# Performance work log

Measured on AMD Instinct MI355X. Metric: run time of the kernel, lower is better.

Reference implementation:

```python
import jax, jax.numpy as jnp
import numpy as np
import math

E = 64    # d_model = 2*feats
FF = 16   # dim_feedforward
F = 32    # feats
W = 100   # window_size
B = 128   # batch
NH = 32   # nhead = feats


def _mha(q_in, kv_in, w_qkv, b_qkv, w_o, b_o):
    # PyTorch nn.MultiheadAttention, seq-first layout [L, B, E]
    wq, wk, wv = jnp.split(w_qkv, 3, axis=0)
    bq, bk, bv = jnp.split(b_qkv, 3)
    q = q_in @ wq.T + bq
    k = kv_in @ wk.T + bk
    v = kv_in @ wv.T + bv
    L, Bb, _ = q.shape
    S = k.shape[0]
    hd = E // NH  # head_dim = 2
    qh = q.reshape(L, Bb, NH, hd)
    kh = k.reshape(S, Bb, NH, hd)
    vh = v.reshape(S, Bb, NH, hd)
    scores = jnp.einsum('lbhd,sbhd->bhls', qh, kh) / math.sqrt(hd)
    attn = jax.nn.softmax(scores, axis=-1)
    out = jnp.einsum('bhls,sbhd->lbhd', attn, vh).reshape(L, Bb, E)
    return out @ w_o.T + b_o


def _ffn(x, w1, b1, w2, b2):
    h = x @ w1.T + b1
    # nn.LeakyReLU(True) => negative_slope=True==1.0 => identity activation
    return h @ w2.T + b2


def _pos_encode(x):
    # pe[t,d] = sin(t*div[d]) + cos(t*div[d])  (both added, as in source)
    div = jnp.exp(jnp.arange(E, dtype=x.dtype) * (-math.log(10000.0) / E))
    pos = jnp.arange(x.shape[0], dtype=x.dtype)[:, None]
    pe = jnp.sin(pos * div) + jnp.cos(pos * div)  # [W, E]
    return x + pe[:, None, :]


def _encode(src, c, tgt, enc_p):
    (qkv_w, qkv_b, out_w, out_b, l1_w, l1_b, l2_w, l2_b) = enc_p
    s = jnp.concatenate([src, c], axis=2) * math.sqrt(F)
    s = _pos_encode(s)
    s = s + _mha(s, s, qkv_w, qkv_b, out_w, out_b)
    s = s + _ffn(s, l1_w, l1_b, l2_w, l2_b)
    t = jnp.tile(tgt, (1, 1, 2))
    return t, s


def _decode(t, mem, dec_p):
    (sa_qkv_w, sa_qkv_b, sa_out_w, sa_out_b,
     ca_qkv_w, ca_qkv_b, ca_out_w, ca_out_b,
     l1_w, l1_b, l2_w, l2_b) = dec_p
    t = t + _mha(t, t, sa_qkv_w, sa_qkv_b, sa_out_w, sa_out_b)
    t = t + _mha(t, mem, ca_qkv_w, ca_qkv_b, ca_out_w, ca_out_b)
    t = t + _ffn(t, l1_w, l1_b, l2_w, l2_b)
    return t


def _forward(src, tgt,
             enc_qkv_w, enc_qkv_b, enc_out_w, enc_out_b, enc_l1_w, enc_l1_b, enc_l2_w, enc_l2_b,
             d1_sa_qkv_w, d1_sa_qkv_b, d1_sa_out_w, d1_sa_out_b,
             d1_ca_qkv_w, d1_ca_qkv_b, d1_ca_out_w, d1_ca_out_b,
             d1_l1_w, d1_l1_b, d1_l2_w, d1_l2_b,
             d2_sa_qkv_w, d2_sa_qkv_b, d2_sa_out_w, d2_sa_out_b,
             d2_ca_qkv_w, d2_ca_qkv_b, d2_ca_out_w, d2_ca_out_b,
             d2_l1_w, d2_l1_b, d2_l2_w, d2_l2_b,
             fcn_w, fcn_b):
    enc_p = (enc_qkv_w, enc_qkv_b, enc_out_w, enc_out_b, enc_l1_w, enc_l1_b, enc_l2_w, enc_l2_b)
    d1_p = (d1_sa_qkv_w, d1_sa_qkv_b, d1_sa_out_w, d1_sa_out_b,
            d1_ca_qkv_w, d1_ca_qkv_b, d1_ca_out_w, d1_ca_out_b,
            d1_l1_w, d1_l1_b, d1_l2_w, d1_l2_b)
    d2_p = (d2_sa_qkv_w, d2_sa_qkv_b, d2_sa_out_w, d2_sa_out_b,
            d2_ca_qkv_w, d2_ca_qkv_b, d2_ca_out_w, d2_ca_out_b,
            d2_l1_w, d2_l1_b, d2_l2_w, d2_l2_b)
    fcn = lambda x: jax.nn.sigmoid(x @ fcn_w.T + fcn_b)

    c = jnp.zeros_like(src)
    t, mem = _encode(src, c, tgt, enc_p)
    x1 = fcn(_decode(t, mem, d1_p))
    c = (x1 - src) ** 2
    t, mem = _encode(src, c, tgt, enc_p)
    x2 = fcn(_decode(t, mem, d2_p))
    return x1, x2


def setup_inputs() -> dict:
    keys = jax.random.split(jax.random.key(0), 40)
    ki = iter(keys)

    def rn(shape, s=0.05):
        return jax.random.normal(next(ki), shape, dtype=jnp.float32) * s

    inp = {}
    inp['src'] = jax.random.normal(next(ki), (W, B, F), dtype=jnp.float32)
    inp['tgt'] = jax.random.normal(next(ki), (W, B, F), dtype=jnp.float32)
    for pfx in ['enc_', 'd1_sa_', 'd1_ca_', 'd2_sa_', 'd2_ca_']:
        inp[pfx + 'qkv_w'] = rn((3 * E, E))
        inp[pfx + 'qkv_b'] = rn((3 * E,))
        inp[pfx + 'out_w'] = rn((E, E))
        inp[pfx + 'out_b'] = rn((E,))
    for pfx in ['enc_', 'd1_', 'd2_']:
        inp[pfx + 'l1_w'] = rn((FF, E))
        inp[pfx + 'l1_b'] = rn((FF,))
        inp[pfx + 'l2_w'] = rn((E, FF))
        inp[pfx + 'l2_b'] = rn((E,))
    inp['fcn_w'] = rn((F, E))
    inp['fcn_b'] = rn((F,))
    return inp


def reference(src, tgt,
              enc_qkv_w, enc_qkv_b, enc_out_w, enc_out_b, enc_l1_w, enc_l1_b, enc_l2_w, enc_l2_b,
              d1_sa_qkv_w, d1_sa_qkv_b, d1_sa_out_w, d1_sa_out_b,
              d1_ca_qkv_w, d1_ca_qkv_b, d1_ca_out_w, d1_ca_out_b,
              d1_l1_w, d1_l1_b, d1_l2_w, d1_l2_b,
              d2_sa_qkv_w, d2_sa_qkv_b, d2_sa_out_w, d2_sa_out_b,
              d2_ca_qkv_w, d2_ca_qkv_b, d2_ca_out_w, d2_ca_out_b,
              d2_l1_w, d2_l1_b, d2_l2_w, d2_l2_b,
              fcn_w, fcn_b):
    return _forward(src, tgt,
                    enc_qkv_w, enc_qkv_b, enc_out_w, enc_out_b, enc_l1_w, enc_l1_b, enc_l2_w, enc_l2_b,
                    d1_sa_qkv_w, d1_sa_qkv_b, d1_sa_out_w, d1_sa_out_b,
                    d1_ca_qkv_w, d1_ca_qkv_b, d1_ca_out_w, d1_ca_out_b,
                    d1_l1_w, d1_l1_b, d1_l2_w, d1_l2_b,
                    d2_sa_qkv_w, d2_sa_qkv_b, d2_sa_out_w, d2_sa_out_b,
                    d2_ca_qkv_w, d2_ca_qkv_b, d2_ca_out_w, d2_ca_out_b,
                    d2_l1_w, d2_l1_b, d2_l2_w, d2_l2_b,
                    fcn_w, fcn_b)
```

## Files before the change

kernel.cpp:

```cpp
#include <hip/hip_runtime.h>
#include <math.h>


#define TPB 1024
#define RH 50
#define SQ32 5.656854249492381f

#ifndef __has_builtin
#define __has_builtin(x) 0
#endif
#if __has_builtin(__builtin_amdgcn_exp2f)
#define EXP2(x) __builtin_amdgcn_exp2f(x)
#else
#define EXP2(x) exp2f(x)
#endif

typedef float v2f __attribute__((ext_vector_type(2)));
typedef float v4f __attribute__((ext_vector_type(4)));

struct KParams { const void* p[36]; };

template<int K, int MC, int WP>
__device__ __forceinline__ void ldwp(const float* __restrict__ Wt, float* __restrict__ Ws,
                                     int moff, int tid)
{
    for (int i = tid; i < MC * K; i += TPB) {
        int m = i / K, k = i - m * K;
        Ws[k * WP + moff + m] = Wt[i];
    }
}

template<int K, int WP>
__device__ __forceinline__ void gemm_dual24(const float* __restrict__ x0,
                                            const float* __restrict__ x1,
                                            const float* __restrict__ w, v2f acc[4])
{
#pragma unroll 4
    for (int kk = 0; kk < K / 4; ++kk) {
        v4f xa = *reinterpret_cast<const v4f*>(x0 + 4 * kk);
        v4f xb = *reinterpret_cast<const v4f*>(x1 + 4 * kk);
#pragma unroll
        for (int j = 0; j < 4; ++j) {
            v4f wv = *reinterpret_cast<const v4f*>(w + (size_t)(4 * kk + j) * WP);
            v2f xj = {xa[j], xb[j]};
#pragma unroll
            for (int c = 0; c < 4; ++c) {
                v2f wc = {wv[c], wv[c]};
                acc[c] = __builtin_elementwise_fma(xj, wc, acc[c]);
            }
        }
    }
}

template<int K, int WP>
__device__ __forceinline__ void gemm14v(const float* __restrict__ x,
                                        const float* __restrict__ w, float acc[4])
{
#pragma unroll 4
    for (int kk = 0; kk < K / 4; ++kk) {
        v4f xv = *reinterpret_cast<const v4f*>(x + 4 * kk);
#pragma unroll
        for (int j = 0; j < 4; ++j) {
            v4f wv = *reinterpret_cast<const v4f*>(w + (size_t)(4 * kk + j) * WP);
#pragma unroll
            for (int c = 0; c < 4; ++c) acc[c] = fmaf(xv[j], wv[c], acc[c]);
        }
    }
}

__device__ __forceinline__ void kv_gemm(const float* __restrict__ Xkv,
    const float* __restrict__ RW, const float* __restrict__ Bqkv,
    int b, int base, float4* __restrict__ KVs, float4* __restrict__ Gx, int tid)
{
    if (tid >= 800) return;
    const int isV = tid >= 400;
    const int u = tid - (isV ? 400 : 0);
    const int r0 = u >> 4, cg = u & 15;
    v2f acc[4] = {};
    gemm_dual24<64, 132>(Xkv + r0 * 68, Xkv + (r0 + 25) * 68,
                         RW + (isV ? 64 : 0) + 4 * cg, acc);
    v4f bb = *reinterpret_cast<const v4f*>(Bqkv + (isV ? 128 : 64) + 4 * cg);
    const int h0 = 2 * cg;
    const int off = isV ? 2 : 0;
#pragma unroll
    for (int rr = 0; rr < 2; ++rr) {
        int sg = base + r0 + 25 * rr;
        v2f p0 = {acc[0][rr] + bb[0], acc[1][rr] + bb[1]};
        v2f p1 = {acc[2][rr] + bb[2], acc[3][rr] + bb[3]};
        *reinterpret_cast<v2f*>(reinterpret_cast<float*>(KVs + h0 * 101 + sg) + off) = p0;
        *reinterpret_cast<v2f*>(reinterpret_cast<float*>(KVs + (h0 + 1) * 101 + sg) + off) = p1;
        float* g0 = reinterpret_cast<float*>(Gx + ((size_t)b * 100 + sg) * 32 + h0) + off;
        float* g1 = reinterpret_cast<float*>(Gx + ((size_t)b * 100 + sg) * 32 + h0 + 1) + off;
        asm volatile("global_store_dwordx2 %0, %1, off sc0 sc1" :: "v"(g0), "v"(p0) : "memory");
        asm volatile("global_store_dwordx2 %0, %1, off sc0 sc1" :: "v"(g1), "v"(p1) : "memory");
    }
}

__device__ __forceinline__ void flag_pub(int* flagme, int st, int tid)
{
    asm volatile("s_waitcnt vmcnt(0)" ::: "memory");
    __syncthreads();
    if (tid == 0)
        asm volatile("global_store_dword %0, %1, off sc0 sc1" :: "v"(flagme), "v"(st) : "memory");
}

__device__ __forceinline__ void q_gemm(const float* __restrict__ Xq,
    const float* __restrict__ RW, const float* __restrict__ Bqkv,
    float* __restrict__ Q, int tid)
{
    if (tid >= 400) return;
    const int r0 = tid >> 4, cg = tid & 15;
    v2f acc[4] = {};
    gemm_dual24<64, 132>(Xq + r0 * 68, Xq + (r0 + 25) * 68, RW + 4 * cg, acc);
    v4f bb = *reinterpret_cast<const v4f*>(Bqkv + 4 * cg);
#pragma unroll
    for (int rr = 0; rr < 2; ++rr)
        *reinterpret_cast<v4f*>(Q + (r0 + 25 * rr) * 68 + 4 * cg) =
            (v4f){acc[0][rr] + bb[0], acc[1][rr] + bb[1],
                  acc[2][rr] + bb[2], acc[3][rr] + bb[3]};
}

__device__ __forceinline__ void kv_wait(const int* flagpt, int st,
    const float4* __restrict__ Gx, int b, int pbase,
    float4* __restrict__ KVs, int tid)
{
    if (tid == 0) {
        int f;
        for (;;) {
            asm volatile("global_load_dword %0, %1, off sc0 sc1\n\ts_waitcnt vmcnt(0)"
                         : "=v"(f) : "v"(flagpt) : "memory");
            if (f >= st) break;
            __builtin_amdgcn_s_sleep(8);
        }
    }
    __syncthreads();
    for (int i = tid; i < 1600; i += TPB) {
        int sl = i >> 5, h = i & 31;
        int sg = pbase + sl;
        const float4* gp = Gx + ((size_t)b * 100 + sg) * 32 + h;
        v4f v;
        asm volatile("global_load_dwordx4 %0, %1, off sc0 sc1\n\ts_waitcnt vmcnt(0)"
                     : "=v"(v) : "v"(gp) : "memory");
        *reinterpret_cast<v4f*>(KVs + h * 101 + sg) = v;
    }
    __syncthreads();
}

__device__ __forceinline__ void attn_block(float* __restrict__ Q,
                                           const float4* __restrict__ KVs, int tid)
{
    if (tid < 416) {
        const int h = tid / 13;
        const int g = tid - 13 * h;
        const int lq0 = 4 * g;
        const float4* kv = KVs + h * 101;
        const float SCALE = 0.7071067811865476f * 1.4426950408889634f;
        float q0[4], q1[4];
#pragma unroll
        for (int j = 0; j < 4; ++j) {
            if (lq0 + j < RH) {
                float2 qv = *reinterpret_cast<const float2*>(Q + (lq0 + j) * 68 + 2 * h);
                q0[j] = qv.x * SCALE; q1[j] = qv.y * SCALE;
            } else { q0[j] = 0.f; q1[j] = 0.f; }
        }
        float mx[4] = {-1e30f, -1e30f, -1e30f, -1e30f};
#pragma unroll 4
        for (int s = 0; s < 100; ++s) {
            float4 k = kv[s];
#pragma unroll
            for (int j = 0; j < 4; ++j)
                mx[j] = fmaxf(mx[j], fmaf(q0[j], k.x, q1[j] * k.y));
        }
        float sum[4] = {0, 0, 0, 0}, a0[4] = {0, 0, 0, 0}, a1[4] = {0, 0, 0, 0};
#pragma unroll 4
        for (int s = 0; s < 100; ++s) {
            float4 k = kv[s];
#pragma unroll
            for (int j = 0; j < 4; ++j) {
                float e = EXP2(fmaf(q0[j], k.x, fmaf(q1[j], k.y, -mx[j])));
                sum[j] += e;
                a0[j] = fmaf(e, k.z, a0[j]);
                a1[j] = fmaf(e, k.w, a1[j]);
            }
        }
#pragma unroll
        for (int j = 0; j < 4; ++j) {
            if (lq0 + j < RH) {
                float inv = 1.f / sum[j];
                *reinterpret_cast<float2*>(Q + (lq0 + j) * 68 + 2 * h) =
                    make_float2(a0[j] * inv, a1[j] * inv);
            }
        }
    }
}

__device__ __forceinline__ void out_res(const float* __restrict__ Ain,
    const float* __restrict__ RW, const float* __restrict__ Bi,
    float* __restrict__ Sres, int tid)
{
    if (tid >= 400) return;
    const int r0 = tid >> 4, cg = tid & 15;
    v2f acc[4] = {};
    gemm_dual24<64, 132>(Ain + r0 * 68, Ain + (r0 + 25) * 68, RW + 4 * cg, acc);
    v4f bb = *reinterpret_cast<const v4f*>(Bi + 4 * cg);
#pragma unroll
    for (int rr = 0; rr < 2; ++rr) {
        float* sp = Sres + (r0 + 25 * rr) * 68 + 4 * cg;
        v4f s0 = *reinterpret_cast<v4f*>(sp);
        *reinterpret_cast<v4f*>(sp) =
            (v4f){acc[0][rr] + bb[0] + s0[0], acc[1][rr] + bb[1] + s0[1],
                  acc[2][rr] + bb[2] + s0[2], acc[3][rr] + bb[3] + s0[3]};
    }
}

__global__ __launch_bounds__(TPB) void k_fused(KParams prm, float* __restrict__ outp,
    float4* __restrict__ kvx0, float4* __restrict__ kvx1, int* __restrict__ flags)
{
    __shared__ float R0[RH * 68];
    __shared__ float R1[RH * 68];
    __shared__ float R3[RH * 68];
    __shared__ float4 KVs[32 * 101];
    __shared__ float RW[64 * 132];
    __shared__ float Hs[RH * 20];
    __shared__ float X1s[RH * 36];

    const int tid = threadIdx.x;
    const int b = blockIdx.x & 127;
    const int half = blockIdx.x >> 7;
    const int base = half * RH;
    const int pbase = RH - base;
    int* flagme = flags + (b * 2 + half) * 32;
    int* flagpt = flags + (b * 2 + 1 - half) * 32;

    const float* src = (const float*)prm.p[0];
    const float* tgt = (const float*)prm.p[1];

#define ATT_STAGE(Xq, Xkv, WQKV, BQ, WOUT, BO, SRES, st)                     \
    {                                                                        \
        float4* Gx = ((st) & 1) ? kvx1 : kvx0;                               \
        __syncthreads();                             \
        ldwp<64, 64, 132>((WQKV) + 4096, RW, 0, tid);           \
        ldwp<64, 64, 132>((WQKV) + 8192, RW, 64, tid);          \
        __syncthreads();                                                     \
        kv_gemm(Xkv, RW, BQ, b, base, KVs, Gx, tid);                         \
        flag_pub(flagme, st, tid);               \
        ldwp<64, 64, 132>(WQKV, RW, 0, tid);                    \
        __syncthreads();                                                     \
        q_gemm(Xq, RW, BQ, R1, tid);                                         \
        kv_wait(flagpt, st, Gx, b, pbase, KVs, tid);                         \
        attn_block(R1, KVs, tid);                                            \
        __syncthreads();                                                     \
        ldwp<64, 64, 132>(WOUT, RW, 0, tid);                                 \
        __syncthreads();                                                     \
        out_res(R1, RW, BO, SRES, tid);                                      \
    }

#define FFN_STAGE(X, W1, B1, W2, B2)                                         \
    {                                                                        \
        __syncthreads();                               \
        ldwp<64, 16, 20>(W1, RW, 0, tid);                                    \
        __syncthreads();                                                     \
        if (tid < 200) {                                                     \
            const int r = tid >> 2, c4 = tid & 3;                            \
            float a[4] = {0, 0, 0, 0};                                       \
            gemm14v<64, 20>((X) + r * 68, RW + 4 * c4, a);                   \
            v4f bb = *reinterpret_cast<const v4f*>((B1) + 4 * c4);           \
            *reinterpret_cast<v4f*>(Hs + r * 20 + 4 * c4) =                  \
                (v4f){a[0] + bb[0], a[1] + bb[1], a[2] + bb[2], a[3] + bb[3]}; \
        }                                                                    \
        __syncthreads();                                                     \
        ldwp<16, 64, 68>(W2, RW, 0, tid);                                    \
        __syncthreads();                                                     \
        if (tid < 400) {                                                     \
            const int r0 = tid >> 4, cg = tid & 15;                          \
            v2f acc[4] = {};                                                 \
            gemm_dual24<16, 68>(Hs + r0 * 20, Hs + (r0 + 25) * 20,           \
                                RW + 4 * cg, acc);                           \
            v4f bb = *reinterpret_cast<const v4f*>((B2) + 4 * cg);           \
            _Pragma("unroll")                                                \
            for (int rr = 0; rr < 2; ++rr) {                                 \
                float* xp = (X) + (r0 + 25 * rr) * 68 + 4 * cg;              \
                v4f u = *reinterpret_cast<v4f*>(xp);                         \
                *reinterpret_cast<v4f*>(xp) =                                \
                    (v4f){acc[0][rr] + bb[0] + u[0], acc[1][rr] + bb[1] + u[1], \
                          acc[2][rr] + bb[2] + u[2], acc[3][rr] + bb[3] + u[3]}; \
            }                                                                \
        }                                                                    \
        __syncthreads();                                                     \
    }

    for (int pass = 0; pass < 2; ++pass) {
        const float* Wq_enc = (const float*)prm.p[2];
        const float* Beq    = (const float*)prm.p[3];
        const float* Wo_enc = (const float*)prm.p[4];
        const float* Beo    = (const float*)prm.p[5];
        const float* Wel1   = (const float*)prm.p[22];
        const float* Bel1   = (const float*)prm.p[23];
        const float* Wel2   = (const float*)prm.p[24];
        const float* Bel2   = (const float*)prm.p[25];
        const float* Wsa    = (const float*)prm.p[pass ? 14 : 6];
        const float* Bsa    = (const float*)prm.p[pass ? 15 : 7];
        const float* Wsao   = (const float*)prm.p[pass ? 16 : 8];
        const float* Bsao   = (const float*)prm.p[pass ? 17 : 9];
        const float* Wca    = (const float*)prm.p[pass ? 18 : 10];
        const float* Bca    = (const float*)prm.p[pass ? 19 : 11];
        const float* Wcao   = (const float*)prm.p[pass ? 20 : 12];
        const float* Bcao   = (const float*)prm.p[pass ? 21 : 13];
        const float* Wdl1   = (const float*)prm.p[pass ? 30 : 26];
        const float* Bdl1   = (const float*)prm.p[pass ? 31 : 27];
        const float* Wdl2   = (const float*)prm.p[pass ? 32 : 28];
        const float* Bdl2   = (const float*)prm.p[pass ? 33 : 29];
        const float* Wf     = (const float*)prm.p[34];
        const float* Bf     = (const float*)prm.p[35];
        float* outx = outp + (pass ? 409600 : 0);

        __syncthreads();
        for (int i = tid; i < RH * 64; i += TPB) {
            int l = i >> 6, d = i & 63;
            int lg = base + l;
            float sv = src[((size_t)lg * 128 + b) * 32 + (d & 31)];
            float v;
            if (d < 32) v = sv;
            else if (pass == 0) v = 0.f;
            else { float df = X1s[l * 36 + (d - 32)] - sv; v = df * df; }
            float div = __expf((float)d * -0.14391156831212787f);
            float pe = 1.4142135623730951f * __sinf((float)lg * div + 0.7853981633974483f);
            R0[l * 68 + d] = v * SQ32 + pe;
        }
        for (int i = tid; i < RH * 8; i += TPB) {
            int l = i >> 3, q4 = i & 7;
            int lg = base + l;
            float4 tv = *reinterpret_cast<const float4*>(tgt + ((size_t)lg * 128 + b) * 32 + 4 * q4);
            *reinterpret_cast<float4*>(R3 + l * 68 + 4 * q4) = tv;
            *reinterpret_cast<float4*>(R3 + l * 68 + 32 + 4 * q4) = tv;
        }

        ATT_STAGE(R0, R0, Wq_enc, Beq, Wo_enc, Beo, R0, pass * 3 + 1)
        FFN_STAGE(R0, Wel1, Bel1, Wel2, Bel2)

        ATT_STAGE(R3, R3, Wsa, Bsa, Wsao, Bsao, R3, pass * 3 + 2)

        ATT_STAGE(R3, R0, Wca, Bca, Wcao, Bcao, R3, pass * 3 + 3)
        FFN_STAGE(R3, Wdl1, Bdl1, Wdl2, Bdl2)

        ldwp<64, 32, 36>(Wf, RW, 0, tid);
        __syncthreads();
        if (tid < 400) {
            const int r = tid >> 3, lp = tid & 7;
            float a[4] = {0, 0, 0, 0};
            gemm14v<64, 36>(R3 + r * 68, RW + 4 * lp, a);
            v4f bb = *reinterpret_cast<const v4f*>(Bf + 4 * lp);
            v4f o;
#pragma unroll
            for (int c = 0; c < 4; ++c) o[c] = 1.f / (1.f + __expf(-(a[c] + bb[c])));
            int rg = base + r;
            *reinterpret_cast<v4f*>(outx + ((size_t)rg * 128 + b) * 32 + 4 * lp) = o;
            if (pass == 0)
                *reinterpret_cast<v4f*>(X1s + r * 36 + 4 * lp) = o;
        }
    }
#undef ATT_STAGE
#undef FFN_STAGE
}

extern "C" void kernel_launch(void* const* d_in, const int* in_sizes, int n_in,
                              void* d_out, int out_size, void* d_ws, size_t ws_size,
                              hipStream_t stream)
{
    KParams prm;
    for (int i = 0; i < 36; ++i) prm.p[i] = d_in[i];
    float4* kvx0 = (float4*)d_ws;
    float4* kvx1 = kvx0 + 409600;
    int* flags = (int*)(kvx1 + 409600);
    k_fused<<<dim3(256), dim3(TPB), 0, stream>>>(prm, (float*)d_out, kvx0, kvx1, flags);
}
```

Measured before the change: 188.3 us.

## Triple-buffer shared weight tiles to overlap weight staging with compute

Replaces the single shared weight buffer with three rotating buffers. The next stage's weights are loaded into a free buffer while the current GEMM or attention step runs, which removes many __syncthreads barriers and serialized load phases. The KV gather in kv_wait now issues both global loads before a single wait instead of waiting after each load. Shared memory use per block rises, and the buffer rotation must be tracked by hand across stages.

```diff
diff --git a/kernel.cpp b/kernel.cpp
--- a/kernel.cpp
+++ b/kernel.cpp
@@ -5,6 +5,9 @@
 #define TPB 1024
 #define RH 50
 #define SQ32 5.656854249492381f
+
+typedef float v2f __attribute__((ext_vector_type(2)));
+typedef float v4f __attribute__((ext_vector_type(4)));
 
 #ifndef __has_builtin
 #define __has_builtin(x) 0
@@ -15,18 +18,14 @@
 #define EXP2(x) exp2f(x)
 #endif
 
-typedef float v2f __attribute__((ext_vector_type(2)));
-typedef float v4f __attribute__((ext_vector_type(4)));
-
 struct KParams { const void* p[36]; };
 
 template<int K, int MC, int WP>
-__device__ __forceinline__ void ldwp(const float* __restrict__ Wt, float* __restrict__ Ws,
-                                     int moff, int tid)
+__device__ __forceinline__ void ldwp(const float* __restrict__ Wt, float* __restrict__ Ws, int tid)
 {
     for (int i = tid; i < MC * K; i += TPB) {
         int m = i / K, k = i - m * K;
-        Ws[k * WP + moff + m] = Wt[i];
+        Ws[k * WP + m] = Wt[i];
     }
 }
 
@@ -69,16 +68,17 @@
 }
 
 __device__ __forceinline__ void kv_gemm(const float* __restrict__ Xkv,
-    const float* __restrict__ RW, const float* __restrict__ Bqkv,
-    int b, int base, float4* __restrict__ KVs, float4* __restrict__ Gx, int tid)
+    const float* __restrict__ BK, const float* __restrict__ BV,
+    const float* __restrict__ Bqkv, int b, int base,
+    float4* __restrict__ KVs, float4* __restrict__ Gx, int tid)
 {
     if (tid >= 800) return;
     const int isV = tid >= 400;
     const int u = tid - (isV ? 400 : 0);
     const int r0 = u >> 4, cg = u & 15;
     v2f acc[4] = {};
-    gemm_dual24<64, 132>(Xkv + r0 * 68, Xkv + (r0 + 25) * 68,
-                         RW + (isV ? 64 : 0) + 4 * cg, acc);
+    gemm_dual24<64, 68>(Xkv + r0 * 68, Xkv + (r0 + 25) * 68,
+                        (isV ? BV : BK) + 4 * cg, acc);
     v4f bb = *reinterpret_cast<const v4f*>(Bqkv + (isV ? 128 : 64) + 4 * cg);
     const int h0 = 2 * cg;
     const int off = isV ? 2 : 0;
@@ -105,13 +105,13 @@
 }
 
 __device__ __forceinline__ void q_gemm(const float* __restrict__ Xq,
-    const float* __restrict__ RW, const float* __restrict__ Bqkv,
+    const float* __restrict__ BW, const float* __restrict__ Bqkv,
     float* __restrict__ Q, int tid)
 {
     if (tid >= 400) return;
     const int r0 = tid >> 4, cg = tid & 15;
     v2f acc[4] = {};
-    gemm_dual24<64, 132>(Xq + r0 * 68, Xq + (r0 + 25) * 68, RW + 4 * cg, acc);
+    gemm_dual24<64, 68>(Xq + r0 * 68, Xq + (r0 + 25) * 68, BW + 4 * cg, acc);
     v4f bb = *reinterpret_cast<const v4f*>(Bqkv + 4 * cg);
 #pragma unroll
     for (int rr = 0; rr < 2; ++rr)
@@ -134,15 +134,18 @@
         }
     }
     __syncthreads();
-    for (int i = tid; i < 1600; i += TPB) {
-        int sl = i >> 5, h = i & 31;
-        int sg = pbase + sl;
-        const float4* gp = Gx + ((size_t)b * 100 + sg) * 32 + h;
-        v4f v;
-        asm volatile("global_load_dwordx4 %0, %1, off sc0 sc1\n\ts_waitcnt vmcnt(0)"
-                     : "=v"(v) : "v"(gp) : "memory");
-        *reinterpret_cast<v4f*>(KVs + h * 101 + sg) = v;
-    }
+    const int i2 = tid + 1024;
+    v4f a1, a2;
+    const float4* p1 = Gx + ((size_t)b * 100 + pbase + (tid >> 5)) * 32 + (tid & 31);
+    asm volatile("global_load_dwordx4 %0, %1, off sc0 sc1" : "=v"(a1) : "v"(p1) : "memory");
+    if (i2 < 1600) {
+        const float4* p2 = Gx + ((size_t)b * 100 + pbase + (i2 >> 5)) * 32 + (i2 & 31);
+        asm volatile("global_load_dwordx4 %0, %1, off sc0 sc1" : "=v"(a2) : "v"(p2) : "memory");
+    }
+    asm volatile("s_waitcnt vmcnt(0)" ::: "memory");
+    *reinterpret_cast<v4f*>(KVs + (tid & 31) * 101 + pbase + (tid >> 5)) = a1;
+    if (i2 < 1600)
+        *reinterpret_cast<v4f*>(KVs + (i2 & 31) * 101 + pbase + (i2 >> 5)) = a2;
     __syncthreads();
 }
 
@@ -195,13 +198,13 @@
 }
 
 __device__ __forceinline__ void out_res(const float* __restrict__ Ain,
-    const float* __restrict__ RW, const float* __restrict__ Bi,
+    const float* __restrict__ BW, const float* __restrict__ Bi,
     float* __restrict__ Sres, int tid)
 {
     if (tid >= 400) return;
     const int r0 = tid >> 4, cg = tid & 15;
     v2f acc[4] = {};
-    gemm_dual24<64, 132>(Ain + r0 * 68, Ain + (r0 + 25) * 68, RW + 4 * cg, acc);
+    gemm_dual24<64, 68>(Ain + r0 * 68, Ain + (r0 + 25) * 68, BW + 4 * cg, acc);
     v4f bb = *reinterpret_cast<const v4f*>(Bi + 4 * cg);
 #pragma unroll
     for (int rr = 0; rr < 2; ++rr) {
@@ -220,7 +223,9 @@
     __shared__ float R1[RH * 68];
     __shared__ float R3[RH * 68];
     __shared__ float4 KVs[32 * 101];
-    __shared__ float RW[64 * 132];
+    __shared__ float B0[64 * 68];
+    __shared__ float B1[64 * 68];
+    __shared__ float B2[64 * 68];
     __shared__ float Hs[RH * 20];
     __shared__ float X1s[RH * 36];
 
@@ -234,60 +239,6 @@
 
     const float* src = (const float*)prm.p[0];
     const float* tgt = (const float*)prm.p[1];
-
-#define ATT_STAGE(Xq, Xkv, WQKV, BQ, WOUT, BO, SRES, st)                     \
-    {                                                                        \
-        float4* Gx = ((st) & 1) ? kvx1 : kvx0;                               \
-        __syncthreads();                             \
-        ldwp<64, 64, 132>((WQKV) + 4096, RW, 0, tid);           \
-        ldwp<64, 64, 132>((WQKV) + 8192, RW, 64, tid);          \
-        __syncthreads();                                                     \
-        kv_gemm(Xkv, RW, BQ, b, base, KVs, Gx, tid);                         \
-        flag_pub(flagme, st, tid);               \
-        ldwp<64, 64, 132>(WQKV, RW, 0, tid);                    \
-        __syncthreads();                                                     \
-        q_gemm(Xq, RW, BQ, R1, tid);                                         \
-        kv_wait(flagpt, st, Gx, b, pbase, KVs, tid);                         \
-        attn_block(R1, KVs, tid);                                            \
-        __syncthreads();                                                     \
-        ldwp<64, 64, 132>(WOUT, RW, 0, tid);                                 \
-        __syncthreads();                                                     \
-        out_res(R1, RW, BO, SRES, tid);                                      \
-    }
-
-#define FFN_STAGE(X, W1, B1, W2, B2)                                         \
-    {                                                                        \
-        __syncthreads();                               \
-        ldwp<64, 16, 20>(W1, RW, 0, tid);                                    \
-        __syncthreads();                                                     \
-        if (tid < 200) {                                                     \
-            const int r = tid >> 2, c4 = tid & 3;                            \
-            float a[4] = {0, 0, 0, 0};                                       \
-            gemm14v<64, 20>((X) + r * 68, RW + 4 * c4, a);                   \
-            v4f bb = *reinterpret_cast<const v4f*>((B1) + 4 * c4);           \
-            *reinterpret_cast<v4f*>(Hs + r * 20 + 4 * c4) =                  \
-                (v4f){a[0] + bb[0], a[1] + bb[1], a[2] + bb[2], a[3] + bb[3]}; \
-        }                                                                    \
-        __syncthreads();                                                     \
-        ldwp<16, 64, 68>(W2, RW, 0, tid);                                    \
-        __syncthreads();                                                     \
-        if (tid < 400) {                                                     \
-            const int r0 = tid >> 4, cg = tid & 15;                          \
-            v2f acc[4] = {};                                                 \
-            gemm_dual24<16, 68>(Hs + r0 * 20, Hs + (r0 + 25) * 20,           \
-                                RW + 4 * cg, acc);                           \
-            v4f bb = *reinterpret_cast<const v4f*>((B2) + 4 * cg);           \
-            _Pragma("unroll")                                                \
-            for (int rr = 0; rr < 2; ++rr) {                                 \
-                float* xp = (X) + (r0 + 25 * rr) * 68 + 4 * cg;              \
-                v4f u = *reinterpret_cast<v4f*>(xp);                         \
-                *reinterpret_cast<v4f*>(xp) =                                \
-                    (v4f){acc[0][rr] + bb[0] + u[0], acc[1][rr] + bb[1] + u[1], \
-                          acc[2][rr] + bb[2] + u[2], acc[3][rr] + bb[3] + u[3]}; \
-            }                                                                \
-        }                                                                    \
-        __syncthreads();                                                     \
-    }
 
     for (int pass = 0; pass < 2; ++pass) {
         const float* Wq_enc = (const float*)prm.p[2];
@@ -315,6 +266,7 @@
         float* outx = outp + (pass ? 409600 : 0);
 
         __syncthreads();
+
         for (int i = tid; i < RH * 64; i += TPB) {
             int l = i >> 6, d = i & 63;
             int lg = base + l;
@@ -334,33 +286,125 @@
             *reinterpret_cast<float4*>(R3 + l * 68 + 4 * q4) = tv;
             *reinterpret_cast<float4*>(R3 + l * 68 + 32 + 4 * q4) = tv;
         }
-
-        ATT_STAGE(R0, R0, Wq_enc, Beq, Wo_enc, Beo, R0, pass * 3 + 1)
-        FFN_STAGE(R0, Wel1, Bel1, Wel2, Bel2)
-
-        ATT_STAGE(R3, R3, Wsa, Bsa, Wsao, Bsao, R3, pass * 3 + 2)
-
-        ATT_STAGE(R3, R0, Wca, Bca, Wcao, Bcao, R3, pass * 3 + 3)
-        FFN_STAGE(R3, Wdl1, Bdl1, Wdl2, Bdl2)
-
-        ldwp<64, 32, 36>(Wf, RW, 0, tid);
+        ldwp<64, 64, 68>(Wq_enc + 4096, B0, tid);
+        ldwp<64, 64, 68>(Wq_enc + 8192, B1, tid);
         __syncthreads();
-        if (tid < 400) {
-            const int r = tid >> 3, lp = tid & 7;
-            float a[4] = {0, 0, 0, 0};
-            gemm14v<64, 36>(R3 + r * 68, RW + 4 * lp, a);
-            v4f bb = *reinterpret_cast<const v4f*>(Bf + 4 * lp);
-            v4f o;
-#pragma unroll
-            for (int c = 0; c < 4; ++c) o[c] = 1.f / (1.f + __expf(-(a[c] + bb[c])));
-            int rg = base + r;
-            *reinterpret_cast<v4f*>(outx + ((size_t)rg * 128 + b) * 32 + 4 * lp) = o;
-            if (pass == 0)
-                *reinterpret_cast<v4f*>(X1s + r * 36 + 4 * lp) = o;
-        }
-    }
-#undef ATT_STAGE
-#undef FFN_STAGE
+
+        {
+            int st = pass * 3 + 1;
+            float4* Gx = (st & 1) ? kvx1 : kvx0;
+            kv_gemm(R0, B0, B1, Beq, b, base, KVs, Gx, tid);
+            ldwp<64, 64, 68>(Wq_enc, B2, tid);
+            flag_pub(flagme, st, tid);
+            q_gemm(R0, B2, Beq, R1, tid);
+            ldwp<64, 64, 68>(Wo_enc, B0, tid);
+            kv_wait(flagpt, st, Gx, b, pbase, KVs, tid);
+            attn_block(R1, KVs, tid);
+            ldwp<64, 16, 20>(Wel1, B1, tid);
+            __syncthreads();
+            out_res(R1, B0, Beo, R0, tid);
+            ldwp<16, 64, 68>(Wel2, B2, tid);
+            __syncthreads();
+            if (tid < 200) {
+                const int r = tid >> 2, c4 = tid & 3;
+                float a[4] = {0, 0, 0, 0};
+                gemm14v<64, 20>(R0 + r * 68, B1 + 4 * c4, a);
+                v4f bb = *reinterpret_cast<const v4f*>(Bel1 + 4 * c4);
+                *reinterpret_cast<v4f*>(Hs + r * 20 + 4 * c4) =
+                    (v4f){a[0] + bb[0], a[1] + bb[1], a[2] + bb[2], a[3] + bb[3]};
+            }
+            ldwp<64, 64, 68>(Wsa + 4096, B0, tid);
+            __syncthreads();
+            if (tid < 400) {
+                const int r0 = tid >> 4, cg = tid & 15;
+                v2f acc[4] = {};
+                gemm_dual24<16, 68>(Hs + r0 * 20, Hs + (r0 + 25) * 20, B2 + 4 * cg, acc);
+                v4f bb = *reinterpret_cast<const v4f*>(Bel2 + 4 * cg);
+#pragma unroll
+                for (int rr = 0; rr < 2; ++rr) {
+                    float* xp = R0 + (r0 + 25 * rr) * 68 + 4 * cg;
+                    v4f u = *reinterpret_cast<v4f*>(xp);
+                    *reinterpret_cast<v4f*>(xp) =
+                        (v4f){acc[0][rr] + bb[0] + u[0], acc[1][rr] + bb[1] + u[1],
+                              acc[2][rr] + bb[2] + u[2], acc[3][rr] + bb[3] + u[3]};
+                }
+            }
+            ldwp<64, 64, 68>(Wsa + 8192, B1, tid);
+            __syncthreads();
+        }
+
+        {
+            int st = pass * 3 + 2;
+            float4* Gx = (st & 1) ? kvx1 : kvx0;
+            kv_gemm(R3, B0, B1, Bsa, b, base, KVs, Gx, tid);
+            ldwp<64, 64, 68>(Wsa, B2, tid);
+            flag_pub(flagme, st, tid);
+            q_gemm(R3, B2, Bsa, R1, tid);
+            ldwp<64, 64, 68>(Wsao, B0, tid);
+            kv_wait(flagpt, st, Gx, b, pbase, KVs, tid);
+            attn_block(R1, KVs, tid);
+            ldwp<64, 64, 68>(Wca + 4096, B1, tid);
+            __syncthreads();
+            out_res(R1, B0, Bsao, R3, tid);
+            ldwp<64, 64, 68>(Wca + 8192, B2, tid);
+            __syncthreads();
+        }
+
+        {
+            int st = pass * 3 + 3;
+            float4* Gx = (st & 1) ? kvx1 : kvx0;
+            kv_gemm(R0, B1, B2, Bca, b, base, KVs, Gx, tid);
+            ldwp<64, 64, 68>(Wca, B0, tid);
+            flag_pub(flagme, st, tid);
+            q_gemm(R3, B0, Bca, R1, tid);
+            ldwp<64, 64, 68>(Wcao, B1, tid);
+            kv_wait(flagpt, st, Gx, b, pbase, KVs, tid);
+            attn_block(R1, KVs, tid);
+            ldwp<64, 16, 20>(Wdl1, B2, tid);
+            __syncthreads();
+            out_res(R1, B1, Bcao, R3, tid);
+            ldwp<16, 64, 68>(Wdl2, B0, tid);
+            __syncthreads();
+            if (tid < 200) {
+                const int r = tid >> 2, c4 = tid & 3;
+                float a[4] = {0, 0, 0, 0};
+                gemm14v<64, 20>(R3 + r * 68, B2 + 4 * c4, a);
+                v4f bb = *reinterpret_cast<const v4f*>(Bdl1 + 4 * c4);
+                *reinterpret_cast<v4f*>(Hs + r * 20 + 4 * c4) =
+                    (v4f){a[0] + bb[0], a[1] + bb[1], a[2] + bb[2], a[3] + bb[3]};
+            }
+            ldwp<64, 32, 36>(Wf, B1, tid);
+            __syncthreads();
+            if (tid < 400) {
+                const int r0 = tid >> 4, cg = tid & 15;
+                v2f acc[4] = {};
+                gemm_dual24<16, 68>(Hs + r0 * 20, Hs + (r0 + 25) * 20, B0 + 4 * cg, acc);
+                v4f bb = *reinterpret_cast<const v4f*>(Bdl2 + 4 * cg);
+#pragma unroll
+                for (int rr = 0; rr < 2; ++rr) {
+                    float* xp = R3 + (r0 + 25 * rr) * 68 + 4 * cg;
+                    v4f u = *reinterpret_cast<v4f*>(xp);
+                    *reinterpret_cast<v4f*>(xp) =
+                        (v4f){acc[0][rr] + bb[0] + u[0], acc[1][rr] + bb[1] + u[1],
+                              acc[2][rr] + bb[2] + u[2], acc[3][rr] + bb[3] + u[3]};
+                }
+            }
+            __syncthreads();
+            if (tid < 400) {
+                const int r = tid >> 3, lp = tid & 7;
+                float a[4] = {0, 0, 0, 0};
+                gemm14v<64, 36>(R3 + r * 68, B1 + 4 * lp, a);
+                v4f bb = *reinterpret_cast<const v4f*>(Bf + 4 * lp);
+                v4f o;
+#pragma unroll
+                for (int c = 0; c < 4; ++c) o[c] = 1.f / (1.f + __expf(-(a[c] + bb[c])));
+                int rg = base + r;
+                *reinterpret_cast<v4f*>(outx + ((size_t)rg * 128 + b) * 32 + 4 * lp) = o;
+                if (pass == 0)
+                    *reinterpret_cast<v4f*>(X1s + r * 36 + 4 * lp) = o;
+            }
+        }
+    }
 }
 
 extern "C" void kernel_launch(void* const* d_in, const int* in_sizes, int n_in,
```

After: 196.0 us. 4.1% more time.

## Split attention keys across thread pairs and widen FFN1 thread mapping

Applied to the files above, without the earlier changes.

Attention now uses 832 threads, with each pair splitting the 100 keys into two halves and merging the partial max, sum and accumulators through xor-shuffle with an online-softmax rescale. The KV gather issues both global loads before a single wait instead of waiting after each load. The first FFN GEMM moves from 200 threads with four outputs each to 800 threads with one output each. The goal is more parallelism and less serial latency per block, at the cost of extra shuffles, exp2 calls and less register reuse per thread.

```diff
diff --git a/kernel.cpp b/kernel.cpp
--- a/kernel.cpp
+++ b/kernel.cpp
@@ -134,26 +134,30 @@
         }
     }
     __syncthreads();
-    for (int i = tid; i < 1600; i += TPB) {
-        int sl = i >> 5, h = i & 31;
-        int sg = pbase + sl;
-        const float4* gp = Gx + ((size_t)b * 100 + sg) * 32 + h;
-        v4f v;
-        asm volatile("global_load_dwordx4 %0, %1, off sc0 sc1\n\ts_waitcnt vmcnt(0)"
-                     : "=v"(v) : "v"(gp) : "memory");
-        *reinterpret_cast<v4f*>(KVs + h * 101 + sg) = v;
-    }
+    const int i2 = tid + 1024;
+    v4f a1, a2;
+    const float4* p1 = Gx + ((size_t)b * 100 + pbase + (tid >> 5)) * 32 + (tid & 31);
+    asm volatile("global_load_dwordx4 %0, %1, off sc0 sc1" : "=v"(a1) : "v"(p1) : "memory");
+    if (i2 < 1600) {
+        const float4* p2 = Gx + ((size_t)b * 100 + pbase + (i2 >> 5)) * 32 + (i2 & 31);
+        asm volatile("global_load_dwordx4 %0, %1, off sc0 sc1" : "=v"(a2) : "v"(p2) : "memory");
+    }
+    asm volatile("s_waitcnt vmcnt(0)" ::: "memory");
+    *reinterpret_cast<v4f*>(KVs + (tid & 31) * 101 + pbase + (tid >> 5)) = a1;
+    if (i2 < 1600)
+        *reinterpret_cast<v4f*>(KVs + (i2 & 31) * 101 + pbase + (i2 >> 5)) = a2;
     __syncthreads();
 }
 
 __device__ __forceinline__ void attn_block(float* __restrict__ Q,
                                            const float4* __restrict__ KVs, int tid)
 {
-    if (tid < 416) {
-        const int h = tid / 13;
-        const int g = tid - 13 * h;
+    if (tid < 832) {
+        const int u = tid >> 1, sh = tid & 1;
+        const int h = u / 13;
+        const int g = u - 13 * h;
         const int lq0 = 4 * g;
-        const float4* kv = KVs + h * 101;
+        const float4* kv = KVs + h * 101 + sh * 50;
         const float SCALE = 0.7071067811865476f * 1.4426950408889634f;
         float q0[4], q1[4];
 #pragma unroll
@@ -164,16 +168,16 @@
             } else { q0[j] = 0.f; q1[j] = 0.f; }
         }
         float mx[4] = {-1e30f, -1e30f, -1e30f, -1e30f};
-#pragma unroll 4
-        for (int s = 0; s < 100; ++s) {
+#pragma unroll 5
+        for (int s = 0; s < 50; ++s) {
             float4 k = kv[s];
 #pragma unroll
             for (int j = 0; j < 4; ++j)
                 mx[j] = fmaxf(mx[j], fmaf(q0[j], k.x, q1[j] * k.y));
         }
         float sum[4] = {0, 0, 0, 0}, a0[4] = {0, 0, 0, 0}, a1[4] = {0, 0, 0, 0};
-#pragma unroll 4
-        for (int s = 0; s < 100; ++s) {
+#pragma unroll 5
+        for (int s = 0; s < 50; ++s) {
             float4 k = kv[s];
 #pragma unroll
             for (int j = 0; j < 4; ++j) {
@@ -185,10 +189,19 @@
         }
 #pragma unroll
         for (int j = 0; j < 4; ++j) {
-            if (lq0 + j < RH) {
-                float inv = 1.f / sum[j];
+            float mo = __shfl_xor(mx[j], 1);
+            float so = __shfl_xor(sum[j], 1);
+            float ao = __shfl_xor(a0[j], 1);
+            float bo = __shfl_xor(a1[j], 1);
+            float m = fmaxf(mx[j], mo);
+            float c1 = EXP2(mx[j] - m), c2 = EXP2(mo - m);
+            float S = fmaf(sum[j], c1, so * c2);
+            float A = fmaf(a0[j], c1, ao * c2);
+            float B = fmaf(a1[j], c1, bo * c2);
+            if (sh == 0 && lq0 + j < RH) {
+                float inv = 1.f / S;
                 *reinterpret_cast<float2*>(Q + (lq0 + j) * 68 + 2 * h) =
-                    make_float2(a0[j] * inv, a1[j] * inv);
+                    make_float2(A * inv, B * inv);
             }
         }
     }
@@ -260,13 +273,18 @@
         __syncthreads();                               \
         ldwp<64, 16, 20>(W1, RW, 0, tid);                                    \
         __syncthreads();                                                     \
-        if (tid < 200) {                                                     \
-            const int r = tid >> 2, c4 = tid & 3;                            \
-            float a[4] = {0, 0, 0, 0};                                       \
-            gemm14v<64, 20>((X) + r * 68, RW + 4 * c4, a);                   \
-            v4f bb = *reinterpret_cast<const v4f*>((B1) + 4 * c4);           \
-            *reinterpret_cast<v4f*>(Hs + r * 20 + 4 * c4) =                  \
-                (v4f){a[0] + bb[0], a[1] + bb[1], a[2] + bb[2], a[3] + bb[3]}; \
+        if (tid < 800) {                \
+            const int r = tid >> 4, c = tid & 15;                            \
+            float a = (B1)[c];                                               \
+            const float* xrow = (X) + r * 68;                                \
+            _Pragma("unroll 4")                                              \
+            for (int kk = 0; kk < 16; ++kk) {                                \
+                v4f xv = *reinterpret_cast<const v4f*>(xrow + 4 * kk);       \
+                _Pragma("unroll")                                            \
+                for (int j = 0; j < 4; ++j)                                  \
+                    a = fmaf(xv[j], RW[(4 * kk + j) * 20 + c], a);           \
+            }                                                                \
+            Hs[r * 20 + c] = a;                                              \
         }                                                                    \
         __syncthreads();                                                     \
         ldwp<16, 64, 68>(W2, RW, 0, tid);                                    \
```

Result: faster. 182.6 us (median of 3 runs) (-3.1%).
